# Kernel optimization log

Measured on AMD Instinct MI355X. Metric: run time of the kernel, lower is better.

The kernel has to match this reference:

```python
import jax, jax.numpy as jnp
import numpy as np

B, D, SLOTS, TOPK, CODE, ANCH = 8192, 64, 32, 3, 128, 32
BETA = 0.25  # vq_commitment_beta


def _clinear(zr, zi, Wr, Wi, br, bi):
    # ComplexLinear: real = Wr(zr)-Wi(zi), imag = Wi(zr)+Wr(zi); each nn.Linear carries its own bias
    return (zr @ Wr + br) - (zi @ Wi + bi), (zr @ Wi + bi) + (zi @ Wr + br)


def _layernorm(x, g, b, eps=1e-6):
    m = x.mean(-1, keepdims=True)
    v = ((x - m) ** 2).mean(-1, keepdims=True)  # biased var, as torch LayerNorm
    return (x - m) / jnp.sqrt(v + eps) * g + b


def setup_inputs() -> dict:
    key = jax.random.key(0)
    ks = jax.random.split(key, 16)
    f = jax.random.normal
    s = 0.05
    rng_init = 1.0 / np.sqrt(D)
    return dict(
        curr_r=f(ks[0], (B, D)), curr_i=f(ks[1], (B, D)),
        mem_r=f(ks[2], (B, SLOTS, D)), mem_i=f(ks[3], (B, SLOTS, D)),
        codebook=jax.random.uniform(ks[4], (CODE, 2 * D), minval=-rng_init, maxval=rng_init),
        qkv_Wr=f(ks[5], (3, D, D)) * s, qkv_Wi=f(ks[6], (3, D, D)) * s,
        qkv_br=jnp.zeros((3, D)), qkv_bi=jnp.zeros((3, D)),
        quad_Wr=f(ks[7], (D, D)) * s, quad_Wi=f(ks[8], (D, D)) * s,
        quad_br=jnp.zeros((D,)), quad_bi=jnp.zeros((D,)),
        sens_Wr=f(ks[9], (D, D)) * s, sens_Wi=f(ks[10], (D, D)) * s,
        sens_br=jnp.zeros((D,)), sens_bi=jnp.zeros((D,)),
        vis_palette=f(ks[11], (ANCH, 2 * D)), aud_palette=f(ks[12], (ANCH, 2 * D)),
        gate_W=f(ks[13], (2 * D, 1)) * s, gate_b=jnp.zeros((1,)),
        addr_W=f(ks[14], (2 * D, SLOTS)) * s, addr_b=jnp.zeros((SLOTS,)),
        ln_gamma_r=jnp.ones((D,)), ln_beta_r=jnp.zeros((D,)),
        ln_gamma_i=jnp.ones((D,)), ln_beta_i=jnp.zeros((D,)),
    )


def reference(curr_r, curr_i, mem_r, mem_i, codebook,
              qkv_Wr, qkv_Wi, qkv_br, qkv_bi,
              quad_Wr, quad_Wi, quad_br, quad_bi,
              sens_Wr, sens_Wi, sens_br, sens_bi,
              vis_palette, aud_palette,
              gate_W, gate_b, addr_W, addr_b,
              ln_gamma_r, ln_beta_r, ln_gamma_i, ln_beta_i):
    sg = jax.lax.stop_gradient
    z_flat = jnp.concatenate([curr_r, curr_i], -1)  # [B,2D]

    # ---- EMA_VQ (eval path): argmin codebook lookup + straight-through ----
    d = (z_flat ** 2).sum(1, keepdims=True) + (codebook ** 2).sum(1) - 2.0 * z_flat @ codebook.T
    d = jnp.maximum(d, 0.0)
    indices = jnp.argmin(d, -1)                      # [B]
    z_q = codebook[indices]                          # [B,2D]
    vq_loss = BETA * ((sg(z_q) - z_flat) ** 2).mean(-1)
    z_q = z_flat + sg(z_q - z_flat)
    probs = jnp.zeros((CODE,), z_flat.dtype).at[indices].add(1.0) / B
    norm_entropy = -(probs * jnp.log(probs + 1e-10)).sum() / np.log(CODE)
    vq_r, vq_i = z_q[..., :D], z_q[..., D:]

    # ---- HermitianGating ----
    qr, qi = _clinear(curr_r, curr_i, qkv_Wr[0], qkv_Wi[0], qkv_br[0], qkv_bi[0])
    kr, ki = _clinear(curr_r, curr_i, qkv_Wr[1], qkv_Wi[1], qkv_br[1], qkv_bi[1])
    vr, vi = _clinear(curr_r, curr_i, qkv_Wr[2], qkv_Wi[2], qkv_br[2], qkv_bi[2])
    gate = jax.nn.sigmoid((qr * kr + qi * ki).sum(-1, keepdims=True))
    g_r, g_i = vr * gate, vi * gate

    # ---- AssociativeMemory: softmax read + topk scatter write ----
    sim = jnp.einsum('bsd,bd->bs', mem_r, curr_r) + jnp.einsum('bsd,bd->bs', mem_i, curr_i)
    sim = sim - sg(sim.max(-1, keepdims=True))
    attn = jax.nn.softmax(sim, -1)
    read_r = jnp.einsum('bs,bsd->bd', attn, mem_r)
    read_i = jnp.einsum('bs,bsd->bd', attn, mem_i)
    write_gate = jax.nn.sigmoid(z_flat @ gate_W + gate_b)[:, :, None]  # [B,1,1]
    logits = z_flat @ addr_W + addr_b
    logits = logits - sg(logits.max(-1, keepdims=True))
    ww = jax.nn.softmax(logits, -1)                  # [B,SLOTS]
    slot_entropy = (-(ww * jnp.log(ww + 1e-10)).sum(-1)).mean()
    top_vals, top_idx = jax.lax.top_k(ww, TOPK)
    sparse = jnp.zeros_like(ww).at[jnp.arange(B)[:, None], top_idx].set(top_vals)
    sparse = sparse / (sparse.sum(-1, keepdims=True) + 1e-6)
    eff = write_gate * sparse[..., None]             # [B,SLOTS,1]
    nm_r = jnp.tanh(mem_r + eff * (curr_r[:, None, :] - mem_r))
    nm_i = jnp.tanh(mem_i + eff * (curr_i[:, None, :] - mem_i))
    nm_r = _layernorm(nm_r, ln_gamma_r, ln_beta_r)
    nm_i = _layernorm(nm_i, ln_gamma_i, ln_beta_i)

    # ---- SubmodalityAnchorModule ----
    s_r, s_i = _clinear(curr_r, curr_i, sens_Wr, sens_Wi, sens_br, sens_bi)
    sflat = jnp.concatenate([s_r, s_i], -1)

    def attend(pal):
        sc = sflat @ pal.T
        sc = sc - sg(sc.max(-1, keepdims=True))
        return jax.nn.softmax(sc, -1) @ pal

    vis = attend(vis_palette)
    aud = attend(aud_palette)
    exp_r = vis[..., :D] - aud[..., D:]   # vis_c + i*aud_c
    exp_i = vis[..., D:] + aud[..., :D]

    # ---- QuadratureModule: multiply by i ----
    zr, zi = _clinear(curr_r, curr_i, quad_Wr, quad_Wi, quad_br, quad_bi)
    q_r, q_i = -zi, zr

    combined = jnp.concatenate(
        [vq_r, vq_i, g_r, g_i, read_r, read_i, exp_r, exp_i, q_r, q_i,
         nm_r.reshape(B, -1), nm_i.reshape(B, -1)], -1)  # [B, 10*D + 2*SLOTS*D]
    return combined, vq_loss, indices, slot_entropy, norm_entropy
```

## Files before the change

### kernel.cpp

```cpp
#include <hip/hip_runtime.h>
#include <hip/hip_bf16.h>


#define NROWS 8
#define NBLOCKS 1024
#define RSTRIDE 4736

static constexpr size_t OFF_VQLOSS = 38797312UL;
static constexpr size_t OFF_IDX    = 38805504UL;
static constexpr size_t OFF_SENT   = 38813696UL;
static constexpr size_t OFF_NENT   = 38813697UL;

struct Params {
  const float* curr_r; const float* curr_i;
  const float* mem_r;  const float* mem_i;
  const float* codebook;
  const float* qkv_Wr; const float* qkv_Wi; const float* qkv_br; const float* qkv_bi;
  const float* quad_Wr; const float* quad_Wi; const float* quad_br; const float* quad_bi;
  const float* sens_Wr; const float* sens_Wi; const float* sens_br; const float* sens_bi;
  const float* vis_pal; const float* aud_pal;
  const float* gate_W; const float* gate_b;
  const float* addr_W; const float* addr_b;
  const float* ln_gr; const float* ln_br; const float* ln_gi; const float* ln_bi;
  float* out;
  int* hist;
  float* rowent;
};

__global__ __launch_bounds__(256) void row_main(Params P) {
  const int b = blockIdx.x;
  const int t = threadIdx.x;
  const int lane = t & 63;
  const int wv = t >> 6;

  __shared__ float zr[64], zi[64];
  __shared__ float s_qr[64], s_qi[64], s_kr[64], s_ki[64], s_vr[64], s_vi[64];
  __shared__ float sfl[128];
  __shared__ float s_sp[4][4][64];
  __shared__ float lp[4][32];
  __shared__ float s_eff[32];
  __shared__ float s_sim[32], s_attn[32];
  __shared__ float s_rr[4][8][8], s_ri[4][8][8];
  __shared__ float s_pv[4][32], s_pa[4][32];
  __shared__ float s_pvp[32], s_pap[32];
  __shared__ float s_vo[128], s_ao[128];
  __shared__ float s_wg, s_gate;

  const size_t bb = (size_t)b;
  const int s = t >> 3, k = t & 7, d0 = k * 8;
  const float* mrp = P.mem_r + ((bb * 32 + s) * 64 + d0);
  const float* mip = P.mem_i + ((bb * 32 + s) * 64 + d0);
  float4 a0 = *(const float4*)mrp, a1 = *(const float4*)(mrp + 4);
  float4 b0 = *(const float4*)mip, b1 = *(const float4*)(mip + 4);
  float mr[8] = {a0.x, a0.y, a0.z, a0.w, a1.x, a1.y, a1.z, a1.w};
  float mi[8] = {b0.x, b0.y, b0.z, b0.w, b1.x, b1.y, b1.z, b1.w};

  if (t < 64)       zr[t]      = P.curr_r[bb * 64 + t];
  else if (t < 128) zi[t - 64] = P.curr_i[bb * 64 + (t - 64)];
  __syncthreads();

  float* orow = P.out + bb * RSTRIDE;

  {
    const int j = lane, cl = wv;
    const float *Wr, *Wi, *br_, *bi_;
    if      (cl == 0) { Wr = P.qkv_Wr;        Wi = P.qkv_Wi;        br_ = P.qkv_br;       bi_ = P.qkv_bi;       }
    else if (cl == 1) { Wr = P.qkv_Wr + 4096; Wi = P.qkv_Wi + 4096; br_ = P.qkv_br + 64;  bi_ = P.qkv_bi + 64;  }
    else if (cl == 2) { Wr = P.qkv_Wr + 8192; Wi = P.qkv_Wi + 8192; br_ = P.qkv_br + 128; bi_ = P.qkv_bi + 128; }
    else              { Wr = P.quad_Wr;       Wi = P.quad_Wi;       br_ = P.quad_br;      bi_ = P.quad_bi;      }
    float aRR = 0.f, aRI = 0.f, aIR = 0.f, aII = 0.f;
    for (int d = 0; d < 64; ++d) {
      const float xr = zr[d], xi = zi[d];
      const float wr = Wr[d * 64 + j], wi = Wi[d * 64 + j];
      aRR += xr * wr; aRI += xr * wi; aIR += xi * wr; aII += xi * wi;
    }
    const float oR = (aRR + br_[j]) - (aII + bi_[j]);
    const float oI = (aRI + bi_[j]) + (aIR + br_[j]);
    if      (cl == 0) { s_qr[j] = oR; s_qi[j] = oI; }
    else if (cl == 1) { s_kr[j] = oR; s_ki[j] = oI; }
    else if (cl == 2) { s_vr[j] = oR; s_vi[j] = oI; }
    else              { orow[512 + j] = -oI; orow[576 + j] = oR; }
    float bRR = 0.f, bRI = 0.f, bIR = 0.f, bII = 0.f;
    for (int dd = 0; dd < 16; ++dd) {
      const int d = wv * 16 + dd;
      const float xr = zr[d], xi = zi[d];
      const float wr = P.sens_Wr[d * 64 + j], wi = P.sens_Wi[d * 64 + j];
      bRR += xr * wr; bRI += xr * wi; bIR += xi * wr; bII += xi * wi;
    }
    s_sp[wv][0][j] = bRR; s_sp[wv][1][j] = bRI; s_sp[wv][2][j] = bIR; s_sp[wv][3][j] = bII;
  }
  __syncthreads();

  {
    float sp = 0.f;
    #pragma unroll
    for (int x = 0; x < 8; ++x) sp += mr[x] * zr[d0 + x] + mi[x] * zi[d0 + x];
    sp += __shfl_xor(sp, 1); sp += __shfl_xor(sp, 2); sp += __shfl_xor(sp, 4);
    if (k == 0) s_sim[s] = sp;
  }
  if (t < 128) {
    const int q = t >> 5, l = t & 31;
    const float* zz = (q < 2) ? zr : zi;
    const int zb = (q & 1) * 32;
    float a = 0.f;
    for (int i = 0; i < 32; ++i) a += zz[zb + i] * P.addr_W[(q * 32 + i) * 32 + l];
    lp[q][l] = a;
  } else if (t < 192) {
    const int j = t - 128;
    float tw = zr[j] * P.gate_W[j] + zi[j] * P.gate_W[64 + j];
    #pragma unroll
    for (int m = 1; m <= 32; m <<= 1) tw += __shfl_xor(tw, m);
    if (j == 0) s_wg = tw;
  } else {
    const int j = t - 192;
    float g = s_qr[j] * s_kr[j] + s_qi[j] * s_ki[j];
    #pragma unroll
    for (int m = 1; m <= 32; m <<= 1) g += __shfl_xor(g, m);
    if (j == 0) s_gate = 1.f / (1.f + expf(-g));
  }
  __syncthreads();

  if (t < 32) {
    float v = s_sim[t];
    float mx = v;
    #pragma unroll
    for (int m = 16; m >= 1; m >>= 1) mx = fmaxf(mx, __shfl_xor(mx, m));
    float e = expf(v - mx);
    float sm = e;
    #pragma unroll
    for (int m = 16; m >= 1; m >>= 1) sm += __shfl_xor(sm, m);
    s_attn[t] = e / sm;
  } else if (t >= 64 && t < 96) {
    const int l = t - 64;
    float lg = lp[0][l] + lp[1][l] + lp[2][l] + lp[3][l] + P.addr_b[l];
    float mx = lg;
    #pragma unroll
    for (int m = 16; m >= 1; m >>= 1) mx = fmaxf(mx, __shfl_xor(mx, m));
    float e = expf(lg - mx);
    float sm = e;
    #pragma unroll
    for (int m = 16; m >= 1; m >>= 1) sm += __shfl_xor(sm, m);
    const float w = e / sm;
    float es = -(w * logf(w + 1e-10f));
    #pragma unroll
    for (int m = 16; m >= 1; m >>= 1) es += __shfl_xor(es, m);
    if (l == 0) P.rowent[b] = es;
    const float myw = w;
    bool picked = false;
    float val = w; int idx = l;
    float sumtop = 0.f;
    #pragma unroll
    for (int it = 0; it < 3; ++it) {
      float v2 = val; int i2 = idx;
      #pragma unroll
      for (int m = 16; m >= 1; m >>= 1) {
        float ov = __shfl_xor(v2, m); int oi = __shfl_xor(i2, m);
        if (ov > v2 || (ov == v2 && oi < i2)) { v2 = ov; i2 = oi; }
      }
      sumtop += v2;
      if (l == i2) { picked = true; val = -1e30f; }
    }
    const float wgate = 1.f / (1.f + expf(-(s_wg + P.gate_b[0])));
    s_eff[l] = picked ? wgate * (myw / (sumtop + 1e-6f)) : 0.f;
  } else if (t >= 128 && t < 192) {
    const int j = t - 128;
    const float aRR = s_sp[0][0][j] + s_sp[1][0][j] + s_sp[2][0][j] + s_sp[3][0][j];
    const float aRI = s_sp[0][1][j] + s_sp[1][1][j] + s_sp[2][1][j] + s_sp[3][1][j];
    const float aIR = s_sp[0][2][j] + s_sp[1][2][j] + s_sp[2][2][j] + s_sp[3][2][j];
    const float aII = s_sp[0][3][j] + s_sp[1][3][j] + s_sp[2][3][j] + s_sp[3][3][j];
    const float oR = (aRR + P.sens_br[j]) - (aII + P.sens_bi[j]);
    const float oI = (aRI + P.sens_bi[j]) + (aIR + P.sens_br[j]);
    sfl[j] = oR; sfl[64 + j] = oI;
  }
  __syncthreads();

  const float aw = s_attn[s];
  {
    float pr[8], pi[8];
    #pragma unroll
    for (int x = 0; x < 8; ++x) { pr[x] = aw * mr[x]; pi[x] = aw * mi[x]; }
    #pragma unroll
    for (int m = 8; m <= 32; m <<= 1) {
      #pragma unroll
      for (int x = 0; x < 8; ++x) { pr[x] += __shfl_xor(pr[x], m); pi[x] += __shfl_xor(pi[x], m); }
    }
    if (lane < 8) {
      #pragma unroll
      for (int x = 0; x < 8; ++x) { s_rr[wv][lane][x] = pr[x]; s_ri[wv][lane][x] = pi[x]; }
    }
  }
  {
    const float eff = s_eff[s];
    float nr[8], ni[8];
    #pragma unroll
    for (int x = 0; x < 8; ++x) {
      nr[x] = tanhf(mr[x] + eff * (zr[d0 + x] - mr[x]));
      ni[x] = tanhf(mi[x] + eff * (zi[d0 + x] - mi[x]));
    }
    float sR = 0.f, sI = 0.f;
    #pragma unroll
    for (int x = 0; x < 8; ++x) { sR += nr[x]; sI += ni[x]; }
    sR += __shfl_xor(sR, 1); sR += __shfl_xor(sR, 2); sR += __shfl_xor(sR, 4);
    sI += __shfl_xor(sI, 1); sI += __shfl_xor(sI, 2); sI += __shfl_xor(sI, 4);
    const float mR = sR * (1.f / 64.f), mI = sI * (1.f / 64.f);
    float vR = 0.f, vI = 0.f;
    #pragma unroll
    for (int x = 0; x < 8; ++x) {
      float dr = nr[x] - mR; vR += dr * dr;
      float di = ni[x] - mI; vI += di * di;
    }
    vR += __shfl_xor(vR, 1); vR += __shfl_xor(vR, 2); vR += __shfl_xor(vR, 4);
    vI += __shfl_xor(vI, 1); vI += __shfl_xor(vI, 2); vI += __shfl_xor(vI, 4);
    const float invR = 1.f / sqrtf(vR * (1.f / 64.f) + 1e-6f);
    const float invI = 1.f / sqrtf(vI * (1.f / 64.f) + 1e-6f);
    float oR[8], oI[8];
    #pragma unroll
    for (int x = 0; x < 8; ++x) {
      const int d = d0 + x;
      oR[x] = (nr[x] - mR) * invR * P.ln_gr[d] + P.ln_br[d];
      oI[x] = (ni[x] - mI) * invI * P.ln_gi[d] + P.ln_bi[d];
    }
    *(float4*)&orow[640 + s * 64 + d0]      = make_float4(oR[0], oR[1], oR[2], oR[3]);
    *(float4*)&orow[640 + s * 64 + d0 + 4]  = make_float4(oR[4], oR[5], oR[6], oR[7]);
    *(float4*)&orow[2688 + s * 64 + d0]     = make_float4(oI[0], oI[1], oI[2], oI[3]);
    *(float4*)&orow[2688 + s * 64 + d0 + 4] = make_float4(oI[4], oI[5], oI[6], oI[7]);
  }
  if (t < 128) {
    const int a = t & 31, q = t >> 5;
    float sc = 0.f;
    for (int x = q * 32; x < q * 32 + 32; ++x) sc += sfl[x] * P.vis_pal[a * 128 + x];
    s_pv[q][a] = sc;
  } else {
    const int tt = t - 128, a = tt & 31, q = tt >> 5;
    float sc = 0.f;
    for (int x = q * 32; x < q * 32 + 32; ++x) sc += sfl[x] * P.aud_pal[a * 128 + x];
    s_pa[q][a] = sc;
  }
  __syncthreads();

  if (t < 64) {
    const int kk = t >> 3, xx = t & 7;
    float rv = s_rr[0][kk][xx] + s_rr[1][kk][xx] + s_rr[2][kk][xx] + s_rr[3][kk][xx];
    float iv = s_ri[0][kk][xx] + s_ri[1][kk][xx] + s_ri[2][kk][xx] + s_ri[3][kk][xx];
    orow[256 + t] = rv;
    orow[320 + t] = iv;
  } else if (t >= 128 && t < 160) {
    const int a = t - 128;
    float sc = s_pv[0][a] + s_pv[1][a] + s_pv[2][a] + s_pv[3][a];
    float mx = sc;
    #pragma unroll
    for (int m = 16; m >= 1; m >>= 1) mx = fmaxf(mx, __shfl_xor(mx, m));
    float e = expf(sc - mx);
    float sm = e;
    #pragma unroll
    for (int m = 16; m >= 1; m >>= 1) sm += __shfl_xor(sm, m);
    s_pvp[a] = e / sm;
  } else if (t >= 192 && t < 224) {
    const int a = t - 192;
    float sc = s_pa[0][a] + s_pa[1][a] + s_pa[2][a] + s_pa[3][a];
    float mx = sc;
    #pragma unroll
    for (int m = 16; m >= 1; m >>= 1) mx = fmaxf(mx, __shfl_xor(mx, m));
    float e = expf(sc - mx);
    float sm = e;
    #pragma unroll
    for (int m = 16; m >= 1; m >>= 1) sm += __shfl_xor(sm, m);
    s_pap[a] = e / sm;
  }
  __syncthreads();

  if (t < 128) {
    float v = 0.f;
    for (int a = 0; a < 32; ++a) v += s_pvp[a] * P.vis_pal[a * 128 + t];
    s_vo[t] = v;
  } else {
    const int j = t - 128;
    float v = 0.f;
    for (int a = 0; a < 32; ++a) v += s_pap[a] * P.aud_pal[a * 128 + j];
    s_ao[j] = v;
  }
  if (t < 64)       orow[128 + t] = s_vr[t] * s_gate;
  else if (t < 128) orow[192 + (t - 64)] = s_vi[t - 64] * s_gate;
  __syncthreads();

  if (t < 64)       orow[384 + t] = s_vo[t] - s_ao[64 + t];
  else if (t < 128) orow[448 + (t - 64)] = s_vo[t] + s_ao[t - 64];
}

__global__ __launch_bounds__(256) void vq_kernel(Params P) {
  const int t = threadIdx.x;
  const int bid = blockIdx.x;
  const int lane = t & 63;
  const int wv = t >> 6;

  __shared__ __align__(16) float s_zr[NROWS][64], s_zi[NROWS][64];
  __shared__ double s_cbn[128];
  __shared__ double s_dall[NROWS][256];
  __shared__ float s_vqls[NROWS];
  __shared__ int s_idx[NROWS];

  {
    const float* cr = P.curr_r + (size_t)bid * (NROWS * 64);
    const float* ci = P.curr_i + (size_t)bid * (NROWS * 64);
    float* zr = &s_zr[0][0];
    float* zi = &s_zi[0][0];
    for (int i = t; i < NROWS * 64; i += 256) { zr[i] = cr[i]; zi[i] = ci[i]; }
  }
  {
    const float* cb = P.codebook + (t & 127) * 128 + (t >> 7) * 64;
    double a = 0.0;
    for (int d = 0; d < 64; ++d) { double w = (double)cb[d]; a = fma(w, w, a); }
    s_dall[0][t] = a;
    __syncthreads();
    if (t < 128) s_cbn[t] = s_dall[0][t] + s_dall[0][t + 128];
    __syncthreads();
  }
  {
    const int c = t & 127, h = t >> 7;
    const float* cb = P.codebook + c * 128 + h * 64;
    const float (*zb)[64] = h ? s_zi : s_zr;
    double acc[NROWS];
    #pragma unroll
    for (int r = 0; r < NROWS; ++r) acc[r] = 0.0;
    for (int d = 0; d < 64; ++d) {
      const double w = (double)cb[d];
      #pragma unroll
      for (int r = 0; r < NROWS; ++r) acc[r] = fma(w, (double)zb[r][d], acc[r]);
    }
    #pragma unroll
    for (int r = 0; r < NROWS; ++r) s_dall[r][h * 128 + c] = acc[r];
    __syncthreads();
    #pragma unroll
    for (int rr = 0; rr < 2; ++rr) {
      const int r = wv * 2 + rr;
      const double d0 = s_cbn[lane]      - 2.0 * (s_dall[r][lane]      + s_dall[r][128 + lane]);
      const double d1 = s_cbn[lane + 64] - 2.0 * (s_dall[r][64 + lane] + s_dall[r][192 + lane]);
      double sv = d0; int si = lane;
      if (d1 < sv) { sv = d1; si = lane + 64; }
      #pragma unroll
      for (int m = 1; m <= 32; m <<= 1) {
        double ov = __shfl_xor(sv, m);
        int oi = __shfl_xor(si, m);
        if (ov < sv || (ov == sv && oi < si)) { sv = ov; si = oi; }
      }
      if (lane == 0) { s_idx[r] = si; atomicAdd(&P.hist[si], 1); }
    }
    __syncthreads();
  }
  {
    #pragma unroll
    for (int rr = 0; rr < 2; ++rr) {
      const int r = wv * 2 + rr;
      const float* cb = P.codebook + (size_t)s_idx[r] * 128;
      float d0_ = cb[lane] - s_zr[r][lane];
      float d1_ = cb[64 + lane] - s_zi[r][lane];
      float v = d0_ * d0_ + d1_ * d1_;
      #pragma unroll
      for (int m = 1; m <= 32; m <<= 1) v += __shfl_xor(v, m);
      if (lane == 0) s_vqls[r] = 0.25f * v * (1.0f / 128.0f);
    }
  }
  __syncthreads();
  {
    const int j = t & 63, g = t >> 6;
    #pragma unroll
    for (int rr = 0; rr < 4; ++rr) {
      const int r = (g >> 1) * 4 + rr;
      float* orow = P.out + ((size_t)bid * NROWS + r) * RSTRIDE;
      const float* cb = P.codebook + (size_t)s_idx[r] * 128;
      if ((g & 1) == 0) {
        float z = s_zr[r][j];
        orow[j] = z + (cb[j] - z);
      } else {
        float z = s_zi[r][j];
        orow[64 + j] = z + (cb[64 + j] - z);
      }
    }
  }
  if (t < NROWS) {
    P.out[OFF_VQLOSS + (size_t)bid * NROWS + t] = s_vqls[t];
    P.out[OFF_IDX + (size_t)bid * NROWS + t] = (float)s_idx[t];
  }
}

__global__ __launch_bounds__(256) void finalize_k(const int* hist, const float* rowent,
                                                  float* out) {
  const int t = threadIdx.x;
  __shared__ float red[256];
  float se = 0.f;
  for (int i = t; i < 8192; i += 256) se += rowent[i];
  red[t] = se;
  __syncthreads();
  for (int off = 128; off >= 1; off >>= 1) {
    if (t < off) red[t] += red[t + off];
    __syncthreads();
  }
  if (t == 0) out[OFF_SENT] = red[0] / 8192.0f;
  __syncthreads();
  float ne = 0.f;
  if (t < 128) {
    const float pp = (float)hist[t] / 8192.0f;
    ne = -(pp * logf(pp + 1e-10f));
  }
  red[t] = ne;
  __syncthreads();
  for (int off = 128; off >= 1; off >>= 1) {
    if (t < off) red[t] += red[t + off];
    __syncthreads();
  }
  if (t == 0) out[OFF_NENT] = red[0] / logf(128.0f);
}

extern "C" void kernel_launch(void* const* d_in, const int* in_sizes, int n_in,
                              void* d_out, int out_size, void* d_ws, size_t ws_size,
                              hipStream_t stream) {
  (void)in_sizes; (void)n_in; (void)out_size; (void)ws_size;
  Params P;
  P.curr_r   = (const float*)d_in[0];
  P.curr_i   = (const float*)d_in[1];
  P.mem_r    = (const float*)d_in[2];
  P.mem_i    = (const float*)d_in[3];
  P.codebook = (const float*)d_in[4];
  P.qkv_Wr   = (const float*)d_in[5];
  P.qkv_Wi   = (const float*)d_in[6];
  P.qkv_br   = (const float*)d_in[7];
  P.qkv_bi   = (const float*)d_in[8];
  P.quad_Wr  = (const float*)d_in[9];
  P.quad_Wi  = (const float*)d_in[10];
  P.quad_br  = (const float*)d_in[11];
  P.quad_bi  = (const float*)d_in[12];
  P.sens_Wr  = (const float*)d_in[13];
  P.sens_Wi  = (const float*)d_in[14];
  P.sens_br  = (const float*)d_in[15];
  P.sens_bi  = (const float*)d_in[16];
  P.vis_pal  = (const float*)d_in[17];
  P.aud_pal  = (const float*)d_in[18];
  P.gate_W   = (const float*)d_in[19];
  P.gate_b   = (const float*)d_in[20];
  P.addr_W   = (const float*)d_in[21];
  P.addr_b   = (const float*)d_in[22];
  P.ln_gr    = (const float*)d_in[23];
  P.ln_br    = (const float*)d_in[24];
  P.ln_gi    = (const float*)d_in[25];
  P.ln_bi    = (const float*)d_in[26];
  P.out = (float*)d_out;
  P.hist = (int*)d_ws;
  P.rowent = (float*)((char*)d_ws + 512);

  hipMemsetAsync(d_ws, 0, 512, stream);
  row_main<<<dim3(8192), dim3(256), 0, stream>>>(P);
  vq_kernel<<<dim3(NBLOCKS), dim3(256), 0, stream>>>(P);
  finalize_k<<<dim3(1), dim3(256), 0, stream>>>(P.hist, P.rowent, (float*)d_out);
}
```

Baseline: 252.3 us.

## Fuse VQ and per-row kernels into one launch with block-index dispatch

Merges the separate VQ kernel and the per-row main kernel into a single launch. The first 1024 blocks handle the codebook argmin and the remaining 8192 handle per-row work, with shared memory overlaid in a union. This removes one kernel launch and the tail/drain gap between the two kernels, letting the fp64-heavy VQ blocks overlap with the memory-bound row blocks. The union sizes shared memory to the larger of the two layouts, which may change occupancy for the row blocks.

```diff
diff --git a/kernel.cpp b/kernel.cpp
--- a/kernel.cpp
+++ b/kernel.cpp
@@ -3,7 +3,6 @@
 
 
 #define NROWS 8
-#define NBLOCKS 1024
 #define RSTRIDE 4736
 
 static constexpr size_t OFF_VQLOSS = 38797312UL;
@@ -27,25 +26,124 @@
   float* rowent;
 };
 
-__global__ __launch_bounds__(256) void row_main(Params P) {
-  const int b = blockIdx.x;
+union __align__(16) SharedU {
+  struct {
+    float zr[64], zi[64];
+    float s_qr[64], s_qi[64], s_kr[64], s_ki[64], s_vr[64], s_vi[64];
+    float sfl[128];
+    float s_sp[4][4][64];
+    float lp[4][32];
+    float s_eff[32];
+    float s_sim[32], s_attn[32];
+    float s_rr[4][8][8], s_ri[4][8][8];
+    float s_pv[4][32], s_pa[4][32];
+    float s_pvp[32], s_pap[32];
+    float s_vo[128], s_ao[128];
+    float s_wg, s_gate;
+  } r;
+  struct {
+    float s_zr[NROWS][64], s_zi[NROWS][64];
+    double s_cbn[128];
+    double s_dall[NROWS][256];
+    float s_vqls[NROWS];
+    int s_idx[NROWS];
+  } v;
+};
+
+__global__ __launch_bounds__(256) void main_kernel(Params P) {
+  __shared__ SharedU u;
   const int t = threadIdx.x;
   const int lane = t & 63;
   const int wv = t >> 6;
 
-  __shared__ float zr[64], zi[64];
-  __shared__ float s_qr[64], s_qi[64], s_kr[64], s_ki[64], s_vr[64], s_vi[64];
-  __shared__ float sfl[128];
-  __shared__ float s_sp[4][4][64];
-  __shared__ float lp[4][32];
-  __shared__ float s_eff[32];
-  __shared__ float s_sim[32], s_attn[32];
-  __shared__ float s_rr[4][8][8], s_ri[4][8][8];
-  __shared__ float s_pv[4][32], s_pa[4][32];
-  __shared__ float s_pvp[32], s_pap[32];
-  __shared__ float s_vo[128], s_ao[128];
-  __shared__ float s_wg, s_gate;
-
+  if (blockIdx.x < 1024) {
+    const int bid = blockIdx.x;
+    {
+      const float* cr = P.curr_r + (size_t)bid * (NROWS * 64);
+      const float* ci = P.curr_i + (size_t)bid * (NROWS * 64);
+      float* zr = &u.v.s_zr[0][0];
+      float* zi = &u.v.s_zi[0][0];
+      for (int i = t; i < NROWS * 64; i += 256) { zr[i] = cr[i]; zi[i] = ci[i]; }
+    }
+    {
+      const float* cb = P.codebook + (t & 127) * 128 + (t >> 7) * 64;
+      double a = 0.0;
+      for (int d = 0; d < 64; ++d) { double w = (double)cb[d]; a = fma(w, w, a); }
+      u.v.s_dall[0][t] = a;
+      __syncthreads();
+      if (t < 128) u.v.s_cbn[t] = u.v.s_dall[0][t] + u.v.s_dall[0][t + 128];
+      __syncthreads();
+    }
+    {
+      const int c = t & 127, h = t >> 7;
+      const float* cb = P.codebook + c * 128 + h * 64;
+      const float (*zb)[64] = h ? u.v.s_zi : u.v.s_zr;
+      double acc[NROWS];
+      #pragma unroll
+      for (int r = 0; r < NROWS; ++r) acc[r] = 0.0;
+      for (int d = 0; d < 64; ++d) {
+        const double w = (double)cb[d];
+        #pragma unroll
+        for (int r = 0; r < NROWS; ++r) acc[r] = fma(w, (double)zb[r][d], acc[r]);
+      }
+      #pragma unroll
+      for (int r = 0; r < NROWS; ++r) u.v.s_dall[r][h * 128 + c] = acc[r];
+      __syncthreads();
+      #pragma unroll
+      for (int rr = 0; rr < 2; ++rr) {
+        const int r = wv * 2 + rr;
+        const double d0 = u.v.s_cbn[lane]      - 2.0 * (u.v.s_dall[r][lane]      + u.v.s_dall[r][128 + lane]);
+        const double d1 = u.v.s_cbn[lane + 64] - 2.0 * (u.v.s_dall[r][64 + lane] + u.v.s_dall[r][192 + lane]);
+        double sv = d0; int si = lane;
+        if (d1 < sv) { sv = d1; si = lane + 64; }
+        #pragma unroll
+        for (int m = 1; m <= 32; m <<= 1) {
+          double ov = __shfl_xor(sv, m);
+          int oi = __shfl_xor(si, m);
+          if (ov < sv || (ov == sv && oi < si)) { sv = ov; si = oi; }
+        }
+        if (lane == 0) { u.v.s_idx[r] = si; atomicAdd(&P.hist[si], 1); }
+      }
+      __syncthreads();
+    }
+    {
+      #pragma unroll
+      for (int rr = 0; rr < 2; ++rr) {
+        const int r = wv * 2 + rr;
+        const float* cb = P.codebook + (size_t)u.v.s_idx[r] * 128;
+        float d0_ = cb[lane] - u.v.s_zr[r][lane];
+        float d1_ = cb[64 + lane] - u.v.s_zi[r][lane];
+        float v = d0_ * d0_ + d1_ * d1_;
+        #pragma unroll
+        for (int m = 1; m <= 32; m <<= 1) v += __shfl_xor(v, m);
+        if (lane == 0) u.v.s_vqls[r] = 0.25f * v * (1.0f / 128.0f);
+      }
+    }
+    __syncthreads();
+    {
+      const int j = t & 63, g = t >> 6;
+      #pragma unroll
+      for (int rr = 0; rr < 4; ++rr) {
+        const int r = (g >> 1) * 4 + rr;
+        float* orow = P.out + ((size_t)bid * NROWS + r) * RSTRIDE;
+        const float* cb = P.codebook + (size_t)u.v.s_idx[r] * 128;
+        if ((g & 1) == 0) {
+          float z = u.v.s_zr[r][j];
+          orow[j] = z + (cb[j] - z);
+        } else {
+          float z = u.v.s_zi[r][j];
+          orow[64 + j] = z + (cb[64 + j] - z);
+        }
+      }
+    }
+    if (t < NROWS) {
+      P.out[OFF_VQLOSS + (size_t)bid * NROWS + t] = u.v.s_vqls[t];
+      P.out[OFF_IDX + (size_t)bid * NROWS + t] = (float)u.v.s_idx[t];
+    }
+    return;
+  }
+
+  const int b = blockIdx.x - 1024;
   const size_t bb = (size_t)b;
   const int s = t >> 3, k = t & 7, d0 = k * 8;
   const float* mrp = P.mem_r + ((bb * 32 + s) * 64 + d0);
@@ -55,8 +153,8 @@
   float mr[8] = {a0.x, a0.y, a0.z, a0.w, a1.x, a1.y, a1.z, a1.w};
   float mi[8] = {b0.x, b0.y, b0.z, b0.w, b1.x, b1.y, b1.z, b1.w};
 
-  if (t < 64)       zr[t]      = P.curr_r[bb * 64 + t];
-  else if (t < 128) zi[t - 64] = P.curr_i[bb * 64 + (t - 64)];
+  if (t < 64)       u.r.zr[t]      = P.curr_r[bb * 64 + t];
+  else if (t < 128) u.r.zi[t - 64] = P.curr_i[bb * 64 + (t - 64)];
   __syncthreads();
 
   float* orow = P.out + bb * RSTRIDE;
@@ -70,58 +168,59 @@
     else              { Wr = P.quad_Wr;       Wi = P.quad_Wi;       br_ = P.quad_br;      bi_ = P.quad_bi;      }
     float aRR = 0.f, aRI = 0.f, aIR = 0.f, aII = 0.f;
     for (int d = 0; d < 64; ++d) {
-      const float xr = zr[d], xi = zi[d];
+      const float xr = u.r.zr[d], xi = u.r.zi[d];
       const float wr = Wr[d * 64 + j], wi = Wi[d * 64 + j];
       aRR += xr * wr; aRI += xr * wi; aIR += xi * wr; aII += xi * wi;
     }
     const float oR = (aRR + br_[j]) - (aII + bi_[j]);
     const float oI = (aRI + bi_[j]) + (aIR + br_[j]);
-    if      (cl == 0) { s_qr[j] = oR; s_qi[j] = oI; }
-    else if (cl == 1) { s_kr[j] = oR; s_ki[j] = oI; }
-    else if (cl == 2) { s_vr[j] = oR; s_vi[j] = oI; }
+    if      (cl == 0) { u.r.s_qr[j] = oR; u.r.s_qi[j] = oI; }
+    else if (cl == 1) { u.r.s_kr[j] = oR; u.r.s_ki[j] = oI; }
+    else if (cl == 2) { u.r.s_vr[j] = oR; u.r.s_vi[j] = oI; }
     else              { orow[512 + j] = -oI; orow[576 + j] = oR; }
     float bRR = 0.f, bRI = 0.f, bIR = 0.f, bII = 0.f;
     for (int dd = 0; dd < 16; ++dd) {
       const int d = wv * 16 + dd;
-      const float xr = zr[d], xi = zi[d];
+      const float xr = u.r.zr[d], xi = u.r.zi[d];
       const float wr = P.sens_Wr[d * 64 + j], wi = P.sens_Wi[d * 64 + j];
       bRR += xr * wr; bRI += xr * wi; bIR += xi * wr; bII += xi * wi;
     }
-    s_sp[wv][0][j] = bRR; s_sp[wv][1][j] = bRI; s_sp[wv][2][j] = bIR; s_sp[wv][3][j] = bII;
+    u.r.s_sp[wv][0][j] = bRR; u.r.s_sp[wv][1][j] = bRI;
+    u.r.s_sp[wv][2][j] = bIR; u.r.s_sp[wv][3][j] = bII;
   }
   __syncthreads();
 
   {
     float sp = 0.f;
     #pragma unroll
-    for (int x = 0; x < 8; ++x) sp += mr[x] * zr[d0 + x] + mi[x] * zi[d0 + x];
+    for (int x = 0; x < 8; ++x) sp += mr[x] * u.r.zr[d0 + x] + mi[x] * u.r.zi[d0 + x];
     sp += __shfl_xor(sp, 1); sp += __shfl_xor(sp, 2); sp += __shfl_xor(sp, 4);
-    if (k == 0) s_sim[s] = sp;
+    if (k == 0) u.r.s_sim[s] = sp;
   }
   if (t < 128) {
     const int q = t >> 5, l = t & 31;
-    const float* zz = (q < 2) ? zr : zi;
+    const float* zz = (q < 2) ? u.r.zr : u.r.zi;
     const int zb = (q & 1) * 32;
     float a = 0.f;
     for (int i = 0; i < 32; ++i) a += zz[zb + i] * P.addr_W[(q * 32 + i) * 32 + l];
-    lp[q][l] = a;
+    u.r.lp[q][l] = a;
   } else if (t < 192) {
     const int j = t - 128;
-    float tw = zr[j] * P.gate_W[j] + zi[j] * P.gate_W[64 + j];
+    float tw = u.r.zr[j] * P.gate_W[j] + u.r.zi[j] * P.gate_W[64 + j];
     #pragma unroll
     for (int m = 1; m <= 32; m <<= 1) tw += __shfl_xor(tw, m);
-    if (j == 0) s_wg = tw;
+    if (j == 0) u.r.s_wg = tw;
   } else {
     const int j = t - 192;
-    float g = s_qr[j] * s_kr[j] + s_qi[j] * s_ki[j];
+    float g = u.r.s_qr[j] * u.r.s_kr[j] + u.r.s_qi[j] * u.r.s_ki[j];
     #pragma unroll
     for (int m = 1; m <= 32; m <<= 1) g += __shfl_xor(g, m);
-    if (j == 0) s_gate = 1.f / (1.f + expf(-g));
+    if (j == 0) u.r.s_gate = 1.f / (1.f + expf(-g));
   }
   __syncthreads();
 
   if (t < 32) {
-    float v = s_sim[t];
+    float v = u.r.s_sim[t];
     float mx = v;
     #pragma unroll
     for (int m = 16; m >= 1; m >>= 1) mx = fmaxf(mx, __shfl_xor(mx, m));
@@ -129,10 +228,10 @@
     float sm = e;
     #pragma unroll
     for (int m = 16; m >= 1; m >>= 1) sm += __shfl_xor(sm, m);
-    s_attn[t] = e / sm;
+    u.r.s_attn[t] = e / sm;
   } else if (t >= 64 && t < 96) {
     const int l = t - 64;
-    float lg = lp[0][l] + lp[1][l] + lp[2][l] + lp[3][l] + P.addr_b[l];
+    float lg = u.r.lp[0][l] + u.r.lp[1][l] + u.r.lp[2][l] + u.r.lp[3][l] + P.addr_b[l];
     float mx = lg;
     #pragma unroll
     for (int m = 16; m >= 1; m >>= 1) mx = fmaxf(mx, __shfl_xor(mx, m));
@@ -160,21 +259,21 @@
       sumtop += v2;
       if (l == i2) { picked = true; val = -1e30f; }
     }
-    const float wgate = 1.f / (1.f + expf(-(s_wg + P.gate_b[0])));
-    s_eff[l] = picked ? wgate * (myw / (sumtop + 1e-6f)) : 0.f;
+    const float wgate = 1.f / (1.f + expf(-(u.r.s_wg + P.gate_b[0])));
+    u.r.s_eff[l] = picked ? wgate * (myw / (sumtop + 1e-6f)) : 0.f;
   } else if (t >= 128 && t < 192) {
     const int j = t - 128;
-    const float aRR = s_sp[0][0][j] + s_sp[1][0][j] + s_sp[2][0][j] + s_sp[3][0][j];
-    const float aRI = s_sp[0][1][j] + s_sp[1][1][j] + s_sp[2][1][j] + s_sp[3][1][j];
-    const float aIR = s_sp[0][2][j] + s_sp[1][2][j] + s_sp[2][2][j] + s_sp[3][2][j];
-    const float aII = s_sp[0][3][j] + s_sp[1][3][j] + s_sp[2][3][j] + s_sp[3][3][j];
+    const float aRR = u.r.s_sp[0][0][j] + u.r.s_sp[1][0][j] + u.r.s_sp[2][0][j] + u.r.s_sp[3][0][j];
+    const float aRI = u.r.s_sp[0][1][j] + u.r.s_sp[1][1][j] + u.r.s_sp[2][1][j] + u.r.s_sp[3][1][j];
+    const float aIR = u.r.s_sp[0][2][j] + u.r.s_sp[1][2][j] + u.r.s_sp[2][2][j] + u.r.s_sp[3][2][j];
+    const float aII = u.r.s_sp[0][3][j] + u.r.s_sp[1][3][j] + u.r.s_sp[2][3][j] + u.r.s_sp[3][3][j];
     const float oR = (aRR + P.sens_br[j]) - (aII + P.sens_bi[j]);
     const float oI = (aRI + P.sens_bi[j]) + (aIR + P.sens_br[j]);
-    sfl[j] = oR; sfl[64 + j] = oI;
-  }
-  __syncthreads();
-
-  const float aw = s_attn[s];
+    u.r.sfl[j] = oR; u.r.sfl[64 + j] = oI;
+  }
+  __syncthreads();
+
+  const float aw = u.r.s_attn[s];
   {
     float pr[8], pi[8];
     #pragma unroll
@@ -186,16 +285,16 @@
     }
     if (lane < 8) {
       #pragma unroll
-      for (int x = 0; x < 8; ++x) { s_rr[wv][lane][x] = pr[x]; s_ri[wv][lane][x] = pi[x]; }
+      for (int x = 0; x < 8; ++x) { u.r.s_rr[wv][lane][x] = pr[x]; u.r.s_ri[wv][lane][x] = pi[x]; }
     }
   }
   {
-    const float eff = s_eff[s];
+    const float eff = u.r.s_eff[s];
     float nr[8], ni[8];
     #pragma unroll
     for (int x = 0; x < 8; ++x) {
-      nr[x] = tanhf(mr[x] + eff * (zr[d0 + x] - mr[x]));
-      ni[x] = tanhf(mi[x] + eff * (zi[d0 + x] - mi[x]));
+      nr[x] = tanhf(mr[x] + eff * (u.r.zr[d0 + x] - mr[x]));
+      ni[x] = tanhf(mi[x] + eff * (u.r.zi[d0 + x] - mi[x]));
     }
     float sR = 0.f, sI = 0.f;
     #pragma unroll
@@ -206,8 +305,8 @@
     float vR = 0.f, vI = 0.f;
     #pragma unroll
     for (int x = 0; x < 8; ++x) {
-      float dr = nr[x] - mR; vR += dr * dr;
-      float di = ni[x] - mI; vI += di * di;
+      const float dr = nr[x] - mR; vR += dr * dr;
+      const float di = ni[x] - mI; vI += di * di;
     }
     vR += __shfl_xor(vR, 1); vR += __shfl_xor(vR, 2); vR += __shfl_xor(vR, 4);
     vI += __shfl_xor(vI, 1); vI += __shfl_xor(vI, 2); vI += __shfl_xor(vI, 4);
@@ -228,25 +327,25 @@
   if (t < 128) {
     const int a = t & 31, q = t >> 5;
     float sc = 0.f;
-    for (int x = q * 32; x < q * 32 + 32; ++x) sc += sfl[x] * P.vis_pal[a * 128 + x];
-    s_pv[q][a] = sc;
+    for (int x = q * 32; x < q * 32 + 32; ++x) sc += u.r.sfl[x] * P.vis_pal[a * 128 + x];
+    u.r.s_pv[q][a] = sc;
   } else {
     const int tt = t - 128, a = tt & 31, q = tt >> 5;
     float sc = 0.f;
-    for (int x = q * 32; x < q * 32 + 32; ++x) sc += sfl[x] * P.aud_pal[a * 128 + x];
-    s_pa[q][a] = sc;
+    for (int x = q * 32; x < q * 32 + 32; ++x) sc += u.r.sfl[x] * P.aud_pal[a * 128 + x];
+    u.r.s_pa[q][a] = sc;
   }
   __syncthreads();
 
   if (t < 64) {
     const int kk = t >> 3, xx = t & 7;
-    float rv = s_rr[0][kk][xx] + s_rr[1][kk][xx] + s_rr[2][kk][xx] + s_rr[3][kk][xx];
-    float iv = s_ri[0][kk][xx] + s_ri[1][kk][xx] + s_ri[2][kk][xx] + s_ri[3][kk][xx];
+    const float rv = u.r.s_rr[0][kk][xx] + u.r.s_rr[1][kk][xx] + u.r.s_rr[2][kk][xx] + u.r.s_rr[3][kk][xx];
+    const float iv = u.r.s_ri[0][kk][xx] + u.r.s_ri[1][kk][xx] + u.r.s_ri[2][kk][xx] + u.r.s_ri[3][kk][xx];
     orow[256 + t] = rv;
     orow[320 + t] = iv;
   } else if (t >= 128 && t < 160) {
     const int a = t - 128;
-    float sc = s_pv[0][a] + s_pv[1][a] + s_pv[2][a] + s_pv[3][a];
+    float sc = u.r.s_pv[0][a] + u.r.s_pv[1][a] + u.r.s_pv[2][a] + u.r.s_pv[3][a];
     float mx = sc;
     #pragma unroll
     for (int m = 16; m >= 1; m >>= 1) mx = fmaxf(mx, __shfl_xor(mx, m));
@@ -254,10 +353,10 @@
     float sm = e;
     #pragma unroll
     for (int m = 16; m >= 1; m >>= 1) sm += __shfl_xor(sm, m);
-    s_pvp[a] = e / sm;
+    u.r.s_pvp[a] = e / sm;
   } else if (t >= 192 && t < 224) {
     const int a = t - 192;
-    float sc = s_pa[0][a] + s_pa[1][a] + s_pa[2][a] + s_pa[3][a];
+    float sc = u.r.s_pa[0][a] + u.r.s_pa[1][a] + u.r.s_pa[2][a] + u.r.s_pa[3][a];
     float mx = sc;
     #pragma unroll
     for (int m = 16; m >= 1; m >>= 1) mx = fmaxf(mx, __shfl_xor(mx, m));
@@ -265,122 +364,26 @@
     float sm = e;
     #pragma unroll
     for (int m = 16; m >= 1; m >>= 1) sm += __shfl_xor(sm, m);
-    s_pap[a] = e / sm;
+    u.r.s_pap[a] = e / sm;
   }
   __syncthreads();
 
   if (t < 128) {
     float v = 0.f;
-    for (int a = 0; a < 32; ++a) v += s_pvp[a] * P.vis_pal[a * 128 + t];
-    s_vo[t] = v;
+    for (int a = 0; a < 32; ++a) v += u.r.s_pvp[a] * P.vis_pal[a * 128 + t];
+    u.r.s_vo[t] = v;
   } else {
     const int j = t - 128;
     float v = 0.f;
-    for (int a = 0; a < 32; ++a) v += s_pap[a] * P.aud_pal[a * 128 + j];
-    s_ao[j] = v;
-  }
-  if (t < 64)       orow[128 + t] = s_vr[t] * s_gate;
-  else if (t < 128) orow[192 + (t - 64)] = s_vi[t - 64] * s_gate;
-  __syncthreads();
-
-  if (t < 64)       orow[384 + t] = s_vo[t] - s_ao[64 + t];
-  else if (t < 128) orow[448 + (t - 64)] = s_vo[t] + s_ao[t - 64];
-}
-
-__global__ __launch_bounds__(256) void vq_kernel(Params P) {
-  const int t = threadIdx.x;
-  const int bid = blockIdx.x;
-  const int lane = t & 63;
-  const int wv = t >> 6;
-
-  __shared__ __align__(16) float s_zr[NROWS][64], s_zi[NROWS][64];
-  __shared__ double s_cbn[128];
-  __shared__ double s_dall[NROWS][256];
-  __shared__ float s_vqls[NROWS];
-  __shared__ int s_idx[NROWS];
-
-  {
-    const float* cr = P.curr_r + (size_t)bid * (NROWS * 64);
-    const float* ci = P.curr_i + (size_t)bid * (NROWS * 64);
-    float* zr = &s_zr[0][0];
-    float* zi = &s_zi[0][0];
-    for (int i = t; i < NROWS * 64; i += 256) { zr[i] = cr[i]; zi[i] = ci[i]; }
-  }
-  {
-    const float* cb = P.codebook + (t & 127) * 128 + (t >> 7) * 64;
-    double a = 0.0;
-    for (int d = 0; d < 64; ++d) { double w = (double)cb[d]; a = fma(w, w, a); }
-    s_dall[0][t] = a;
-    __syncthreads();
-    if (t < 128) s_cbn[t] = s_dall[0][t] + s_dall[0][t + 128];
-    __syncthreads();
-  }
-  {
-    const int c = t & 127, h = t >> 7;
-    const float* cb = P.codebook + c * 128 + h * 64;
-    const float (*zb)[64] = h ? s_zi : s_zr;
-    double acc[NROWS];
-    #pragma unroll
-    for (int r = 0; r < NROWS; ++r) acc[r] = 0.0;
-    for (int d = 0; d < 64; ++d) {
-      const double w = (double)cb[d];
-      #pragma unroll
-      for (int r = 0; r < NROWS; ++r) acc[r] = fma(w, (double)zb[r][d], acc[r]);
-    }
-    #pragma unroll
-    for (int r = 0; r < NROWS; ++r) s_dall[r][h * 128 + c] = acc[r];
-    __syncthreads();
-    #pragma unroll
-    for (int rr = 0; rr < 2; ++rr) {
-      const int r = wv * 2 + rr;
-      const double d0 = s_cbn[lane]      - 2.0 * (s_dall[r][lane]      + s_dall[r][128 + lane]);
-      const double d1 = s_cbn[lane + 64] - 2.0 * (s_dall[r][64 + lane] + s_dall[r][192 + lane]);
-      double sv = d0; int si = lane;
-      if (d1 < sv) { sv = d1; si = lane + 64; }
-      #pragma unroll
-      for (int m = 1; m <= 32; m <<= 1) {
-        double ov = __shfl_xor(sv, m);
-        int oi = __shfl_xor(si, m);
-        if (ov < sv || (ov == sv && oi < si)) { sv = ov; si = oi; }
-      }
-      if (lane == 0) { s_idx[r] = si; atomicAdd(&P.hist[si], 1); }
-    }
-    __syncthreads();
-  }
-  {
-    #pragma unroll
-    for (int rr = 0; rr < 2; ++rr) {
-      const int r = wv * 2 + rr;
-      const float* cb = P.codebook + (size_t)s_idx[r] * 128;
-      float d0_ = cb[lane] - s_zr[r][lane];
-      float d1_ = cb[64 + lane] - s_zi[r][lane];
-      float v = d0_ * d0_ + d1_ * d1_;
-      #pragma unroll
-      for (int m = 1; m <= 32; m <<= 1) v += __shfl_xor(v, m);
-      if (lane == 0) s_vqls[r] = 0.25f * v * (1.0f / 128.0f);
-    }
-  }
-  __syncthreads();
-  {
-    const int j = t & 63, g = t >> 6;
-    #pragma unroll
-    for (int rr = 0; rr < 4; ++rr) {
-      const int r = (g >> 1) * 4 + rr;
-      float* orow = P.out + ((size_t)bid * NROWS + r) * RSTRIDE;
-      const float* cb = P.codebook + (size_t)s_idx[r] * 128;
-      if ((g & 1) == 0) {
-        float z = s_zr[r][j];
-        orow[j] = z + (cb[j] - z);
-      } else {
-        float z = s_zi[r][j];
-        orow[64 + j] = z + (cb[64 + j] - z);
-      }
-    }
-  }
-  if (t < NROWS) {
-    P.out[OFF_VQLOSS + (size_t)bid * NROWS + t] = s_vqls[t];
-    P.out[OFF_IDX + (size_t)bid * NROWS + t] = (float)s_idx[t];
-  }
+    for (int a = 0; a < 32; ++a) v += u.r.s_pap[a] * P.aud_pal[a * 128 + j];
+    u.r.s_ao[j] = v;
+  }
+  if (t < 64)       orow[128 + t] = u.r.s_vr[t] * u.r.s_gate;
+  else if (t < 128) orow[192 + (t - 64)] = u.r.s_vi[t - 64] * u.r.s_gate;
+  __syncthreads();
+
+  if (t < 64)       orow[384 + t] = u.r.s_vo[t] - u.r.s_ao[64 + t];
+  else if (t < 128) orow[448 + (t - 64)] = u.r.s_vo[t] + u.r.s_ao[t - 64];
 }
 
 __global__ __launch_bounds__(256) void finalize_k(const int* hist, const float* rowent,
@@ -448,7 +451,6 @@
   P.rowent = (float*)((char*)d_ws + 512);
 
   hipMemsetAsync(d_ws, 0, 512, stream);
-  row_main<<<dim3(8192), dim3(256), 0, stream>>>(P);
-  vq_kernel<<<dim3(NBLOCKS), dim3(256), 0, stream>>>(P);
+  main_kernel<<<dim3(1024 + 8192), dim3(256), 0, stream>>>(P);
   finalize_k<<<dim3(1), dim3(256), 0, stream>>>(P.hist, P.rowent, (float*)d_out);
 }
```

New measurement: 239.9 us. 4.9% less time.
